# Kernel tuning notes

Measured on AMD Instinct MI355X. Metric: run time of the kernel, lower is better.

Reference implementation:

```python
import jax, jax.numpy as jnp
import numpy as np

VR = 8          # voxel_resolution
CLASSES = 40
LO, HI = -2.0, 2.0


def setup_inputs() -> dict:
    key = jax.random.key(0)
    kx, kw, kb = jax.random.split(key, 3)
    B, N = 1024, 8192
    in_dim = VR ** 3
    x = jax.random.normal(kx, (B, N, 3), dtype=jnp.float32)
    W = jax.random.normal(kw, (CLASSES, in_dim), dtype=jnp.float32) / np.sqrt(in_dim)
    b = jax.random.normal(kb, (CLASSES,), dtype=jnp.float32) * 0.01
    return {"x": x, "W": W, "b": b}


def _voxel_counts(x):
    """Fused equivalent of the per-sample torch.histogramdd loop.

    x: (B, N, 3) in [-2, 2]; uniform bins -> direct index arithmetic +
    one segment_sum over all B*N points. Matches torch.histogramdd
    semantics: points outside [LO, HI] are dropped; x == HI falls in the
    last bin. Returns normalized counts (B, VR**3).
    """
    B, N, _ = x.shape
    width = (HI - LO) / VR
    idx = jnp.floor((x - LO) / width).astype(jnp.int32)      # (B, N, 3)
    idx = jnp.minimum(idx, VR - 1)                            # x == HI -> last bin
    valid = jnp.all((x >= LO) & (x <= HI), axis=-1)           # (B, N)
    lin = (idx[..., 0] * VR + idx[..., 1]) * VR + idx[..., 2]  # (B, N)
    seg = jnp.arange(B, dtype=jnp.int32)[:, None] * (VR ** 3) + lin
    # out-of-range points -> segment id beyond num_segments (dropped)
    seg = jnp.where(valid, seg, B * VR ** 3)
    ones = jnp.ones((B, N), dtype=x.dtype)
    counts = jax.ops.segment_sum(ones.reshape(-1), seg.reshape(-1),
                                 num_segments=B * VR ** 3)
    return counts.reshape(B, VR ** 3) / N


def reference(x, W, b):
    counts = _voxel_counts(x)                 # (B, VR**3)
    # mode == "count": use normalized counts as-is
    return counts @ W.T + b                   # (B, classes)
```

## Files before the change

### kernel.cpp

```cpp
#include <hip/hip_runtime.h>


#define VR        8
#define BINS      512
#define CLASSES   40
#define NPTS      8192
#define THREADS   512
#define CHUNK_PTS 2048
#define CHUNK_F4  1536
#define NCHUNK    4

__global__ __launch_bounds__(THREADS, 8) void voxel_cls_kernel(
    const float* __restrict__ x,
    const float* __restrict__ W,
    const float* __restrict__ bias,
    float* __restrict__ out)
{
    __shared__ float xs[CHUNK_PTS * 3];
    __shared__ unsigned int hist[BINS];
    const int t = threadIdx.x;
    const int b = blockIdx.x;

    hist[t] = 0u;

    const float4* px = (const float4*)(x + (size_t)b * NPTS * 3);
    float4* xsv = (float4*)xs;

    float4 r0 = px[t];
    float4 r1 = px[t + 512];
    float4 r2 = px[t + 1024];

    for (int c = 0; c < NCHUNK; ++c) {
        __syncthreads();
        xsv[t]        = r0;
        xsv[t + 512]  = r1;
        xsv[t + 1024] = r2;
        if (c + 1 < NCHUNK) {
            const float4* ns = px + (c + 1) * CHUNK_F4;
            r0 = ns[t]; r1 = ns[t + 512]; r2 = ns[t + 1024];
        }
        __syncthreads();

        #pragma unroll
        for (int k = 0; k < 4; ++k) {
            const int p = k * THREADS + t;
            const float vx = xs[p * 3 + 0];
            const float vy = xs[p * 3 + 1];
            const float vz = xs[p * 3 + 2];
            const bool ok = (__builtin_fabsf(vx) <= 2.f) &&
                            (__builtin_fabsf(vy) <= 2.f) &&
                            (__builtin_fabsf(vz) <= 2.f);
            const int ix = min((int)((vx + 2.f) * 2.f), VR - 1);
            const int iy = min((int)((vy + 2.f) * 2.f), VR - 1);
            const int iz = min((int)((vz + 2.f) * 2.f), VR - 1);
            if (ok) atomicAdd(&hist[(ix * VR + iy) * VR + iz], 1u);
        }
    }
    __syncthreads();

    if (t < CLASSES * 4) {
        const int c = t >> 2;
        const int s = t & 3;
        const float* Wc = W + c * BINS;
        float acc = 0.f;
        #pragma unroll 8
        for (int i = 0; i < BINS / 4; ++i) {
            const int v = i * 4 + s;
            acc += (float)hist[v] * Wc[v];
        }
        acc += __shfl_xor(acc, 1);
        acc += __shfl_xor(acc, 2);
        if (s == 0)
            out[b * CLASSES + c] = acc * (1.0f / NPTS) + bias[c];
    }
}

extern "C" void kernel_launch(void* const* d_in, const int* in_sizes, int n_in,
                              void* d_out, int out_size, void* d_ws, size_t ws_size,
                              hipStream_t stream) {
    const float* x    = (const float*)d_in[0];
    const float* W    = (const float*)d_in[1];
    const float* bias = (const float*)d_in[2];
    float* out        = (float*)d_out;

    const int nbatch = in_sizes[0] / (NPTS * 3);
    voxel_cls_kernel<<<nbatch, THREADS, 0, stream>>>(x, W, bias, out);
}
```

Baseline: 153.7 us.

## Split histogram and matvec into two kernels with shared-memory W tiling

The fused kernel is split in two. The first kernel builds per-sample voxel histograms and writes them to workspace. The second kernel does the matrix-vector product for four samples per block, staging transposed W tiles in shared memory so each W load is reused across samples. This aims to drop the tail of the histogram kernel, where only 160 threads read W from global memory while the other threads sit idle. The cost is an extra kernel launch plus a global round trip for the histograms, about 2 MB.

```diff
diff --git a/kernel.cpp b/kernel.cpp
--- a/kernel.cpp
+++ b/kernel.cpp
@@ -5,16 +5,14 @@
 #define BINS      512
 #define CLASSES   40
 #define NPTS      8192
-#define THREADS   512
+
+#define T1        512
 #define CHUNK_PTS 2048
 #define CHUNK_F4  1536
 #define NCHUNK    4
 
-__global__ __launch_bounds__(THREADS, 8) void voxel_cls_kernel(
-    const float* __restrict__ x,
-    const float* __restrict__ W,
-    const float* __restrict__ bias,
-    float* __restrict__ out)
+__global__ __launch_bounds__(T1, 8) void hist_kernel(
+    const float* __restrict__ x, unsigned int* __restrict__ Hc)
 {
     __shared__ float xs[CHUNK_PTS * 3];
     __shared__ unsigned int hist[BINS];
@@ -43,7 +41,7 @@
 
         #pragma unroll
         for (int k = 0; k < 4; ++k) {
-            const int p = k * THREADS + t;
+            const int p = k * T1 + t;
             const float vx = xs[p * 3 + 0];
             const float vy = xs[p * 3 + 1];
             const float vz = xs[p * 3 + 2];
@@ -57,21 +55,70 @@
         }
     }
     __syncthreads();
+    Hc[(size_t)b * BINS + t] = hist[t];
+}
 
-    if (t < CLASSES * 4) {
-        const int c = t >> 2;
-        const int s = t & 3;
-        const float* Wc = W + c * BINS;
-        float acc = 0.f;
-        #pragma unroll 8
-        for (int i = 0; i < BINS / 4; ++i) {
-            const int v = i * 4 + s;
-            acc += (float)hist[v] * Wc[v];
+#define T2 256
+
+__global__ __launch_bounds__(T2, 1) void matvec_kernel(
+    const unsigned int* __restrict__ Hc,
+    const float* __restrict__ W,
+    const float* __restrict__ bias,
+    float* __restrict__ out)
+{
+    __shared__ float wt[256][CLASSES];
+    __shared__ float hs[4][BINS];
+    const int t = threadIdx.x;
+    const int w = t >> 6;
+    const int l = t & 63;
+    const int r = blockIdx.x * 4 + w;
+
+    {
+        const uint4* h4 = (const uint4*)(Hc + (size_t)r * BINS);
+        float4* hv = (float4*)hs[w];
+        #pragma unroll
+        for (int k = 0; k < 2; ++k) {
+            const uint4 u = h4[l + 64 * k];
+            float4 f;
+            f.x = (float)u.x; f.y = (float)u.y;
+            f.z = (float)u.z; f.w = (float)u.w;
+            hv[l + 64 * k] = f;
         }
-        acc += __shfl_xor(acc, 1);
-        acc += __shfl_xor(acc, 2);
-        if (s == 0)
-            out[b * CLASSES + c] = acc * (1.0f / NPTS) + bias[c];
+    }
+
+    const int c = l;
+    float a0 = 0.f, a1 = 0.f, a2 = 0.f, a3 = 0.f;
+
+    for (int h = 0; h < 2; ++h) {
+        __syncthreads();
+        #pragma unroll
+        for (int i = 0; i < 10; ++i) {
+            const int j  = t + i * T2;
+            const int vl = j / 10;
+            const int q  = j % 10;
+            const int v  = vl + 256 * h;
+            #pragma unroll
+            for (int k = 0; k < 4; ++k)
+                wt[vl][4 * q + k] = W[(4 * q + k) * BINS + v];
+        }
+        __syncthreads();
+
+        if (c < CLASSES) {
+            #pragma unroll 4
+            for (int i = 0; i < 64; ++i) {
+                const int v0 = 4 * i;
+                const int g0 = 256 * h + v0;
+                a0 += hs[w][g0 + 0] * wt[v0 + 0][c];
+                a1 += hs[w][g0 + 1] * wt[v0 + 1][c];
+                a2 += hs[w][g0 + 2] * wt[v0 + 2][c];
+                a3 += hs[w][g0 + 3] * wt[v0 + 3][c];
+            }
+        }
+    }
+
+    if (c < CLASSES) {
+        const float acc = ((a0 + a1) + (a2 + a3));
+        out[r * CLASSES + c] = acc * (1.0f / NPTS) + bias[c];
     }
 }
 
@@ -82,7 +129,9 @@
     const float* W    = (const float*)d_in[1];
     const float* bias = (const float*)d_in[2];
     float* out        = (float*)d_out;
+    unsigned int* Hc  = (unsigned int*)d_ws;
 
     const int nbatch = in_sizes[0] / (NPTS * 3);
-    voxel_cls_kernel<<<nbatch, THREADS, 0, stream>>>(x, W, bias, out);
+    hist_kernel  <<<nbatch,     T1, 0, stream>>>(x, Hc);
+    matvec_kernel<<<nbatch / 4, T2, 0, stream>>>(Hc, W, bias, out);
 }
```

Measured after the change: 161.3 us. 1.05x slower.
